# Kernel tuning notes

Measured on AMD Instinct MI355X. Metric: run time of the kernel, lower is better.

Reference implementation:

```python
import jax, jax.numpy as jnp
import numpy as np

PATCH = 8
EPS = 1e-5

def patch_split(x, s):
    # B C H W -> B s*s rH rW C
    B, C, H, W = x.shape
    rH, rW = H // s, W // s
    out = x.reshape(B, C, s, rH, s, rW)
    out = out.transpose(0, 2, 4, 3, 5, 1)
    return out.reshape(B, s * s, rH, rW, C)

def patch_recover(x, s):
    # B s*s rH rW C -> B C H W
    B, N, rH, rW, C = x.shape
    out = x.reshape(B, s, s, rH, rW, C)
    out = out.transpose(0, 5, 1, 3, 2, 4)
    return out.reshape(B, C, s * rH, s * rW)

def conv2d(x, w, pad):
    return jax.lax.conv_general_dilated(x, w, (1, 1), [(pad, pad), (pad, pad)],
                                        dimension_numbers=('NCHW', 'OIHW', 'NCHW'))

def bn_relu(x, g, b):
    # eval-mode BatchNorm2d with fresh running stats (mean=0, var=1)
    scale = (g / jnp.sqrt(1.0 + EPS))[None, :, None, None]
    return jax.nn.relu(x * scale + b[None, :, None, None])


def setup_inputs() -> dict:
    key = jax.random.key(0)
    ks = jax.random.split(key, 24)
    r = lambda i, shape, s=0.02: jax.random.normal(ks[i], shape, jnp.float32) * s
    B, H, W, C, K, P = 4, 64, 64, 512, 19, 64
    return {
        'M_1': jax.random.normal(ks[0], (B, 2048, H, W), jnp.float32),
        'F': jax.random.normal(ks[1], (B, C, H, W), jnp.float32),
        'I': jax.random.normal(ks[2], (B, K, H, W), jnp.float32),
        'R': jax.random.uniform(ks[3], (B, K, PATCH, PATCH), jnp.float32),
        'lg_w1': r(4, (P, P)), 'lg_w2': r(5, (C, C)),
        'fuse_w': r(6, (P,)), 'fuse_b': r(7, (1,)),
        'q_w': r(8, (256, C)), 'q_b': r(9, (256,)),
        'k_w': r(10, (256, C)), 'k_b': r(11, (256,)),
        'v_w': r(12, (256, C)), 'v_b': r(13, (256,)),
        'c1_w': r(14, (512, 256, 1, 1)),
        'bn1_g': jnp.ones((512,)), 'bn1_b': jnp.zeros((512,)),
        'c2_w': r(15, (512, 512, 3, 3)),
        'bn2_g': jnp.ones((512,)), 'bn2_b': jnp.zeros((512,)),
        'c3_w': r(16, (512, 2560, 3, 3)),
        'bn3_g': jnp.ones((512,)), 'bn3_b': jnp.zeros((512,)),
        'drop_w': r(17, (K, 512, 1, 1)),
    }


def reference(M_1, F, I, R, lg_w1, lg_w2, fuse_w, fuse_b, q_w, q_b, k_w, k_b,
              v_w, v_b, c1_w, bn1_g, bn1_b, c2_w, bn2_g, bn2_b, c3_w, bn3_g,
              bn3_b, drop_w):
    B = F.shape[0]
    F_p5 = patch_split(F, PATCH)          # B P rH rW C
    _, P, rH, rW, C = F_p5.shape
    I_p5 = patch_split(I, PATCH)          # B P rH rW K
    K = I_p5.shape[-1]
    F_p = F_p5.reshape(B, P, rH * rW, C)
    I_p = I_p5.reshape(B, P, rH * rW, K)
    bin_conf = R.reshape(B, K, P).transpose(0, 2, 1)[..., None]  # B P K 1
    pix = jax.nn.softmax(I_p, axis=2)
    F_l = jnp.einsum('bpnk,bpnc->bpkc', pix, F_p) * bin_conf     # B P K C
    # LG block: 1x1 conv over P channels, residual relu, linear over C
    h = jnp.einsum('qp,bpkc->bqkc', lg_w1, F_l)
    h = jax.nn.relu(h + F_l)
    F_l = jnp.einsum('bpkc,dc->bpkd', h, lg_w2)
    # FUSE: 1x1 conv P->1 (with bias); broadcast replaces torch .repeat
    F_g = jnp.einsum('p,bpkc->bkc', fuse_w, F_l) + fuse_b        # B K C
    query = jnp.einsum('bpnc,dc->bpnd', F_p, q_w) + q_b          # B P N 256
    key_ = jnp.einsum('bpkc,dc->bpkd', F_l, k_w) + k_b           # B P K 256
    value = jnp.einsum('bkc,dc->bkd', F_g, v_w) + v_b            # B K 256
    aff = jax.nn.softmax(jnp.einsum('bpnd,bpkd->bpnk', query, key_), axis=-1)
    F_s = jnp.einsum('bpnk,bkd->bpnd', aff, value)               # B P N 256
    F_s = patch_recover(F_s.reshape(B, P, rH, rW, -1), PATCH)    # B 256 H W
    Fo1 = F + bn_relu(conv2d(F_s, c1_w, 0), bn1_g, bn1_b)
    x2 = bn_relu(conv2d(Fo1, c2_w, 1), bn2_g, bn2_b)
    x3 = bn_relu(conv2d(jnp.concatenate([x2, M_1], axis=1), c3_w, 1), bn3_g, bn3_b)
    # Dropout2d is identity in eval; final 1x1 classifier conv
    return conv2d(x3, drop_w, 0)
```

## Files before the change

### kernel.cpp

```cpp
#include <hip/hip_runtime.h>
#include <hip/hip_bf16.h>

typedef __hip_bfloat16 bf16;
using short8 = __attribute__((ext_vector_type(8))) short;
using f32x4  = __attribute__((ext_vector_type(4))) float;

__device__ __forceinline__ float b2f(bf16 v){ return __bfloat162float(v); }
__device__ __forceinline__ bf16  f2b(float v){ return __float2bfloat16(v); }

#define EPSV 1e-5f

__device__ __forceinline__ void gload16(const void* g, void* l) {
  __builtin_amdgcn_global_load_lds(
      (const __attribute__((address_space(1))) unsigned int*)g,
      (__attribute__((address_space(3))) unsigned int*)l, 16, 0, 0);
}

__global__ __launch_bounds__(256) void k_cast(const float* __restrict__ in,
                                              bf16* __restrict__ out, int n4) {
  int i = blockIdx.x * 256 + threadIdx.x;
  if (i < n4) {
    float4 v = ((const float4*)in)[i];
    union { ushort4 u; bf16 h[4]; } o;
    o.h[0] = f2b(v.x); o.h[1] = f2b(v.y); o.h[2] = f2b(v.z); o.h[3] = f2b(v.w);
    ((ushort4*)out)[i] = o.u;
  }
}

__global__ __launch_bounds__(256) void k_wtr(const float* __restrict__ w,
                                             bf16* __restrict__ wt, int CI) {
  int oc = blockIdx.x, c0 = blockIdx.y * 128;
  __shared__ float ld[128 * 9];
  const float* src = w + ((size_t)oc * CI + c0) * 9;
  for (int i = threadIdx.x; i < 128 * 9; i += 256) ld[i] = src[i];
  __syncthreads();
  for (int i = threadIdx.x; i < 128 * 9; i += 256) {
    int k9 = i / 128, t = i - k9 * 128;
    wt[((size_t)k9 * 512 + oc) * CI + c0 + t] = f2b(ld[t * 9 + k9]);
  }
}

__global__ __launch_bounds__(256) void k_m1t(const float* __restrict__ M1,
                                             bf16* __restrict__ M1b) {
  int b = blockIdx.x >> 6, y = blockIdx.x & 63;
  int c0 = blockIdx.y * 64;
  __shared__ float t[64][65];
  for (int i = threadIdx.x; i < 4096; i += 256) {
    int cc = i >> 6, x = i & 63;
    t[x][cc] = M1[((size_t)(b * 2048 + c0 + cc) * 64 + y) * 64 + x];
  }
  __syncthreads();
  for (int i = threadIdx.x; i < 4096; i += 256) {
    int x = i >> 6, cc = i & 63;
    M1b[((size_t)((b * 64 + y) * 64 + x)) * 2048 + c0 + cc] = f2b(t[x][cc]);
  }
}

__global__ __launch_bounds__(256) void k_fp2(const float* __restrict__ F,
                                             bf16* __restrict__ FP) {
  int b = blockIdx.x >> 6, y = blockIdx.x & 63;
  int tid = threadIdx.x;
  __shared__ float t[256][65];
  int p_hi = (y >> 3) << 3, n_hi = (y & 7) << 3;
  for (int half = 0; half < 2; half++) {
    int c0 = half << 8;
    for (int i = tid; i < 256 * 64; i += 256) {
      int cc = i >> 6, x = i & 63;
      t[cc][x] = F[((size_t)(b * 512 + c0 + cc) * 64 + y) * 64 + x];
    }
    __syncthreads();
    for (int x = 0; x < 64; x++) {
      int p = p_hi + (x >> 3), n = n_hi + (x & 7);
      FP[((size_t)(b * 64 + p)) * 32768 + n * 512 + c0 + tid] = f2b(t[tid][x]);
    }
    __syncthreads();
  }
}

__global__ __launch_bounds__(256) void k_flocal2(const float* __restrict__ I,
        const float* __restrict__ R, const bf16* __restrict__ FP,
        float* __restrict__ FL0) {
  int bp = blockIdx.x, b = bp >> 6, p = bp & 63;
  int tid = threadIdx.x, w = tid >> 6, lane = tid & 63;
  __shared__ __align__(16) bf16 fps[64 * 512];
  __shared__ float pix[19][64];
  __shared__ float bc[19];
  {
    const bf16* src = FP + (size_t)bp * 32768 + lane * 8;
    #pragma unroll
    for (int t = 0; t < 16; t++) {
      int chunk = w + t * 4;
      gload16(src + chunk * 512, (char*)fps + chunk * 1024);
    }
  }
  int py = (p >> 3) * 8, px = (p & 7) * 8;
  for (int i = tid; i < 19 * 64; i += 256) {
    int k = i >> 6, n = i & 63;
    int y = py + (n >> 3), x = px + (n & 7);
    pix[k][n] = I[((size_t)(b * 19 + k) * 64 + y) * 64 + x];
  }
  if (tid < 19) bc[tid] = R[(size_t)(b * 19 + tid) * 64 + p];
  __syncthreads();
  if (tid < 19) {
    float mx = -1e30f;
    for (int n = 0; n < 64; n++) mx = fmaxf(mx, pix[tid][n]);
    float s = 0.f;
    for (int n = 0; n < 64; n++) { float e = __expf(pix[tid][n] - mx); pix[tid][n] = e; s += e; }
    float sc = bc[tid] / s;
    for (int n = 0; n < 64; n++) pix[tid][n] *= sc;
  }
  __syncthreads();
  for (int task = tid; task < 19 * 64; task += 256) {
    int k = task >> 6, c8 = (task & 63) << 3;
    float acc[8] = {};
    for (int n = 0; n < 64; n++) {
      float pv = pix[k][n];
      union { short8 s; bf16 h[8]; } v;
      v.s = *(const short8*)&fps[n * 512 + c8];
      #pragma unroll
      for (int j = 0; j < 8; j++) acc[j] += pv * b2f(v.h[j]);
    }
    float* dst = FL0 + ((size_t)(b * 64 + p) * 19 + k) * 512 + c8;
    #pragma unroll
    for (int j = 0; j < 8; j++) dst[j] = acc[j];
  }
}

__global__ __launch_bounds__(256) void k_lg1(const float* __restrict__ FL0,
        const float* __restrict__ w1, bf16* __restrict__ Hb) {
  int tid = threadIdx.x;
  int b = blockIdx.y;
  int n0 = blockIdx.x * 256;
  __shared__ float W[64][64];
  __shared__ float Xs[16][256];
  for (int i = tid; i < 4096; i += 256) W[i >> 6][i & 63] = w1[i];
  float acc[64];
  #pragma unroll
  for (int po = 0; po < 64; po++) acc[po] = 0.f;
  for (int q0 = 0; q0 < 64; q0 += 16) {
    __syncthreads();
    for (int i = tid; i < 4096; i += 256) {
      int q = i >> 8, j = i & 255;
      Xs[q][j] = FL0[(size_t)(b * 64 + q0 + q) * 9728 + n0 + j];
    }
    __syncthreads();
    for (int q = 0; q < 16; q++) {
      float xv = Xs[q][tid];
      #pragma unroll
      for (int po = 0; po < 64; po++) acc[po] += W[po][q0 + q] * xv;
    }
  }
  for (int po = 0; po < 64; po++) {
    float r = acc[po] + FL0[(size_t)(b * 64 + po) * 9728 + n0 + tid];
    Hb[(size_t)(b * 64 + po) * 9728 + n0 + tid] = f2b(fmaxf(r, 0.f));
  }
}

template<int MODE>
__global__ __launch_bounds__(256) void k_gmm(
    const bf16* __restrict__ A, const bf16* __restrict__ B,
    const float* __restrict__ bias, float* __restrict__ C,
    bf16* __restrict__ Cb, int N, int K,
    const float* __restrict__ g, const float* __restrict__ bb,
    const float* __restrict__ Fres, bf16* __restrict__ outb) {
  int tid = threadIdx.x;
  int m0 = blockIdx.x * 128, n0 = blockIdx.y * 128;
  int w = tid >> 6, lane = tid & 63, ln = lane & 15, qd = lane >> 4;
  int wm = w & 1, wn = w >> 1;
  __shared__ __align__(16) char smem[34816];

  f32x4 acc[4][4];
  #pragma unroll
  for (int i = 0; i < 4; i++)
    #pragma unroll
    for (int j = 0; j < 4; j++) acc[i][j] = (f32x4){0.f, 0.f, 0.f, 0.f};

  int rsub = lane >> 2, ch = lane & 3;
  auto stage = [&](int p) {
    char* base = smem + (p & 1) * 16384;
    int k0 = p << 5;
    #pragma unroll
    for (int t = 0; t < 2; t++) {
      int ii = w + t * 4;
      int r = ii * 16 + rsub;
      int sw = (ch ^ ((r >> 1) & 3)) << 3;
      gload16(A + (size_t)(m0 + r) * K + k0 + sw, base + ii * 1024);
      gload16(B + (size_t)(n0 + r) * K + k0 + sw, base + 8192 + ii * 1024);
    }
  };
  auto compute = [&](int p) {
    const char* base = smem + (p & 1) * 16384;
    short8 af[4], bv[4];
    #pragma unroll
    for (int mi = 0; mi < 4; mi++) {
      int r = wm * 64 + mi * 16 + ln;
      af[mi] = *(const short8*)(base + r * 64 + ((qd ^ ((r >> 1) & 3)) << 4));
    }
    #pragma unroll
    for (int ni = 0; ni < 4; ni++) {
      int r = wn * 64 + ni * 16 + ln;
      bv[ni] = *(const short8*)(base + 8192 + r * 64 + ((qd ^ ((r >> 1) & 3)) << 4));
    }
    #pragma unroll
    for (int mi = 0; mi < 4; mi++)
      #pragma unroll
      for (int ni = 0; ni < 4; ni++)
        acc[mi][ni] = __builtin_amdgcn_mfma_f32_16x16x32_bf16(
            af[mi], bv[ni], acc[mi][ni], 0, 0, 0);
  };

  int KT = K >> 5;
  stage(0);
  __syncthreads();
  for (int p = 0; p < KT; p++) {
    if (p + 1 < KT) stage(p + 1);
    compute(p);
    __syncthreads();
  }

  if (MODE <= 1) {
    #pragma unroll
    for (int mi = 0; mi < 4; mi++) {
      #pragma unroll
      for (int r = 0; r < 4; r++) {
        int m = m0 + wm * 64 + mi * 16 + qd * 4 + r;
        #pragma unroll
        for (int ni = 0; ni < 4; ni++) {
          int n = n0 + wn * 64 + ni * 16 + ln;
          float v = acc[mi][ni][r];
          if (bias) v += bias[n];
          C[(size_t)m * N + n] = v;
          if (MODE == 1) Cb[(size_t)m * N + n] = f2b(v);
        }
      }
    }
  } else {
    bf16* EP = (bf16*)smem;
    int b = n0 >> 12;
    #pragma unroll
    for (int mi = 0; mi < 4; mi++) {
      #pragma unroll
      for (int r = 0; r < 4; r++) {
        int ml = wm * 64 + mi * 16 + qd * 4 + r;
        int oc = m0 + ml;
        float sc = g[oc] * rsqrtf(1.f + EPSV);
        float bt = bb[oc];
        #pragma unroll
        for (int ni = 0; ni < 4; ni++) {
          int nl = wn * 64 + ni * 16 + ln;
          int pix = n0 + nl;
          int y = (pix >> 6) & 63, x = pix & 63;
          float v = fmaxf(acc[mi][ni][r] * sc + bt, 0.f)
                  + Fres[((size_t)(b * 512 + oc) * 64 + y) * 64 + x];
          EP[nl * 136 + ml] = f2b(v);
        }
      }
    }
    __syncthreads();
    int pl = tid >> 1, half = tid & 1;
    size_t gb = (size_t)(n0 + pl) * 512 + m0 + half * 64;
    const bf16* row = &EP[pl * 136 + half * 64];
    #pragma unroll
    for (int j2 = 0; j2 < 8; j2++)
      *(short8*)(outb + gb + j2 * 8) = *(const short8*)(row + j2 * 8);
  }
}

__global__ __launch_bounds__(256) void k_fusev(const float* __restrict__ FL,
        const float* __restrict__ fw, const float* __restrict__ fbv,
        const float* __restrict__ vw, const float* __restrict__ vb,
        float* __restrict__ VAL) {
  int tid = threadIdx.x;
  int bk = blockIdx.x, b = bk / 19, k = bk % 19;
  __shared__ float fwl[64];
  __shared__ __align__(16) float fg[512];
  if (tid < 64) fwl[tid] = fw[tid];
  __syncthreads();
  float fbias = fbv[0];
  for (int c = tid; c < 512; c += 256) {
    float s = 0.f;
    for (int p = 0; p < 64; p++)
      s += fwl[p] * FL[((size_t)(b * 64 + p) * 19 + k) * 512 + c];
    fg[c] = s + fbias;
  }
  __syncthreads();
  int d = tid;
  float s = vb[d];
  const float4* vr = (const float4*)(vw + (size_t)d * 512);
  const float4* fr = (const float4*)fg;
  for (int c4 = 0; c4 < 128; c4++) {
    float4 wv = vr[c4], f = fr[c4];
    s += f.x * wv.x + f.y * wv.y + f.z * wv.z + f.w * wv.w;
  }
  VAL[(size_t)bk * 256 + d] = s;
}

__global__ __launch_bounds__(256) void k_attn(const float* __restrict__ Q,
        const float* __restrict__ KEY, const float* __restrict__ VAL,
        bf16* __restrict__ FS) {
  int tid = threadIdx.x;
  int bp = blockIdx.x, b = bp >> 6, p = bp & 63;
  __shared__ __align__(16) float ks[19][256];
  __shared__ __align__(16) float vs[19][256];
  __shared__ float Ss[64][20];
  __shared__ bf16 ot[64][256];
  for (int i = tid; i < 19 * 256; i += 256) {
    ks[i >> 8][i & 255] = KEY[(size_t)bp * 19 * 256 + i];
    vs[i >> 8][i & 255] = VAL[(size_t)b * 19 * 256 + i];
  }
  __syncthreads();
  {
    int n = tid >> 2, kq = tid & 3;
    const float4* qrow = (const float4*)(Q + ((size_t)bp * 64 + n) * 256);
    for (int k = kq; k < 19; k += 4) {
      const float4* kr = (const float4*)&ks[k][0];
      float s = 0.f;
      for (int d4 = 0; d4 < 64; d4++) {
        float4 qv = qrow[d4], kv = kr[d4];
        s += qv.x * kv.x + qv.y * kv.y + qv.z * kv.z + qv.w * kv.w;
      }
      Ss[n][k] = s;
    }
  }
  __syncthreads();
  if (tid < 64) {
    float mx = -1e30f;
    for (int k = 0; k < 19; k++) mx = fmaxf(mx, Ss[tid][k]);
    float sum = 0.f;
    for (int k = 0; k < 19; k++) { float e = __expf(Ss[tid][k] - mx); Ss[tid][k] = e; sum += e; }
    float inv = 1.f / sum;
    for (int k = 0; k < 19; k++) Ss[tid][k] *= inv;
  }
  __syncthreads();
  {
    int d = tid;
    for (int nn = 0; nn < 64; nn++) {
      float s = 0.f;
      #pragma unroll
      for (int k = 0; k < 19; k++) s += Ss[nn][k] * vs[k][d];
      ot[nn][d] = f2b(s);
    }
  }
  __syncthreads();
  {
    int py = (p >> 3) * 8, px = (p & 7) * 8;
    int nn = tid >> 2, q = tid & 3;
    int y = py + (nn >> 3), x = px + (nn & 7);
    size_t gb = (((size_t)(b * 64 + y) * 64) + x) * 256 + q * 64;
    const bf16* row = &ot[nn][q * 64];
    #pragma unroll
    for (int j = 0; j < 8; j++)
      *(short8*)(FS + gb + j * 8) = *(const short8*)(row + j * 8);
  }
}

__global__ __launch_bounds__(256) void k_conv3(
    const bf16* __restrict__ Xin, int Cin,
    const bf16* __restrict__ M1b, const float* __restrict__ M1f, int C2,
    const bf16* __restrict__ WT,
    const float* __restrict__ g, const float* __restrict__ bb,
    bf16* __restrict__ out, int Cos) {
  int tid = threadIdx.x;
  int b = blockIdx.x >> 4, y0 = (blockIdx.x & 15) * 4;
  int oc0 = blockIdx.y * 128;
  int w = tid >> 6, lane = tid & 63, ln = lane & 15, qd = lane >> 4;
  int wocg = w & 1, wyp = w >> 1;
  int Ct = Cin + C2;

  __shared__ __align__(16) char smem[103936];
  char* smA  = smem;
  char* smB  = smem + 49152;
  char* dump = smem + 99840;

  for (int bufi = 0; bufi < 2; bufi++) {
    char* bbuf = smB + bufi * 25344;
    for (int i = tid; i < 6 * 2 * 32; i += 256) {
      int rl = i >> 6, hh = (i >> 5) & 1, kk = i & 31;
      *(bf16*)(bbuf + (rl * 66 + (hh ? 65 : 0)) * 64 + kk * 2) = f2b(0.f);
    }
    if (y0 == 0)
      for (int i = tid; i < 66 * 16; i += 256) ((float*)bbuf)[i] = 0.f;
    if (y0 == 60)
      for (int i = tid; i < 66 * 16; i += 256)
        ((float*)(bbuf + 5 * 66 * 64))[i] = 0.f;
  }

  f32x4 acc[4][8];
  #pragma unroll
  for (int i = 0; i < 4; i++)
    #pragma unroll
    for (int j = 0; j < 8; j++) acc[i][j] = (f32x4){0.f, 0.f, 0.f, 0.f};

  int NPH = (Ct >> 5) * 3;

  auto stageA = [&](int p) {
    int c0 = (p / 3) << 5, ky = p % 3;
    char* base = smA + (p & 1) * 24576;
    int j = w;
    #pragma unroll
    for (int t = 0; t < 6; t++, j += 4) {
      int kx = j >> 3, i8 = j & 7;
      int ocl = i8 * 16 + (lane >> 2);
      const bf16* src = WT + ((size_t)((ky * 3 + kx) * 512 + oc0 + ocl) * Ct + c0)
                      + (((lane & 3) ^ ((ocl >> 1) & 3)) << 3);
      gload16(src, base + (kx * 128 + i8 * 16) * 64);
    }
  };
  auto stageB = [&](int gi) {
    int c0 = gi << 5;
    char* bbuf = smB + (gi & 1) * 25344;
    if (c0 < Cin || M1b != nullptr) {
      const bf16* T; int Cs, cb;
      if (c0 < Cin) { T = Xin; Cs = Cin; cb = c0; }
      else          { T = M1b; Cs = C2;  cb = c0 - Cin; }
      #pragma unroll
      for (int rl = 0; rl < 6; rl++) {
        int yy = y0 + rl - 1;
        bool ok = (unsigned)yy < 64u;
        int yc = ok ? yy : y0;
        int xx = w * 16 + (lane >> 2), xr = xx + 1;
        const bf16* src = T + ((size_t)((b * 64 + yc) * 64 + xx) * Cs + cb)
                        + (((lane & 3) ^ ((xr >> 1) & 3)) << 3);
        char* dst = ok ? (bbuf + (rl * 66 + 1 + w * 16) * 64) : (dump + w * 1024);
        gload16(src, dst);
      }
    } else {
      #pragma unroll
      for (int t = 0; t < 2; t++) {
        int rl = w + t * 4;
        if (rl < 6) {
          int yy = y0 + rl - 1;
          if ((unsigned)yy < 64u) {
            int xx = lane, xr = xx + 1;
            const float* mp = M1f + ((size_t)(b * 2048 + (c0 - Cin)) * 64 + yy) * 64 + xx;
            #pragma unroll
            for (int q = 0; q < 8; q++) {
              union { ushort4 u; bf16 h[4]; } pk;
              #pragma unroll
              for (int jj = 0; jj < 4; jj++) pk.h[jj] = f2b(mp[(size_t)(q * 4 + jj) * 4096]);
              *(ushort4*)(bbuf + (rl * 66 + xr) * 64
                          + ((((q >> 1) ^ ((xr >> 1) & 3)) << 4) | ((q & 1) << 3))) = pk.u;
            }
          }
        }
      }
    }
  };
  auto computeP = [&](int p) {
    int ky = p % 3;
    const char* base = smA + (p & 1) * 24576;
    const char* bB   = smB + ((p / 3) & 1) * 25344;
    int rl0 = 2 * wyp + ky;
    #pragma unroll
    for (int kx = 0; kx < 3; kx++) {
      short8 af[4], bv[8];
      #pragma unroll
      for (int mi = 0; mi < 4; mi++) {
        int ocl = wocg * 64 + mi * 16 + ln;
        af[mi] = *(const short8*)(base + (kx * 128 + ocl) * 64
                                  + ((qd ^ ((ocl >> 1) & 3)) << 4));
      }
      #pragma unroll
      for (int ni = 0; ni < 8; ni++) {
        int rl = rl0 + (ni >> 2);
        int xr = (ni & 3) * 16 + ln + kx;
        bv[ni] = *(const short8*)(bB + (rl * 66 + xr) * 64
                                  + ((qd ^ ((xr >> 1) & 3)) << 4));
      }
      #pragma unroll
      for (int mi = 0; mi < 4; mi++)
        #pragma unroll
        for (int ni = 0; ni < 8; ni++)
          acc[mi][ni] = __builtin_amdgcn_mfma_f32_16x16x32_bf16(
              af[mi], bv[ni], acc[mi][ni], 0, 0, 0);
    }
  };

  stageB(0);
  stageA(0);
  asm volatile("s_waitcnt vmcnt(0)" ::: "memory");
  __syncthreads();

  for (int p = 0; p < NPH; p++) {
    int pn = p + 1;
    bool hasA = pn < NPH;
    bool hasB = hasA && (pn % 3 == 0);
    bool bfast = false;
    if (hasA) stageA(pn);
    if (hasB) {
      int gi = pn / 3;
      bfast = ((gi << 5) < Cin) || (M1b != nullptr);
      stageB(gi);
    }
    __builtin_amdgcn_sched_barrier(0);
    if (!hasA)              asm volatile("s_waitcnt vmcnt(0)"  ::: "memory");
    else if (hasB && bfast) asm volatile("s_waitcnt vmcnt(12)" ::: "memory");
    else                    asm volatile("s_waitcnt vmcnt(6)"  ::: "memory");
    __builtin_amdgcn_s_barrier();
    __builtin_amdgcn_sched_barrier(0);
    computeP(p);
    __builtin_amdgcn_sched_barrier(0);
    asm volatile("s_waitcnt lgkmcnt(0)" ::: "memory");
    __builtin_amdgcn_s_barrier();
  }
  __syncthreads();

  {
    bf16* EP = (bf16*)smem;
    #pragma unroll
    for (int mi = 0; mi < 4; mi++) {
      int oclb = wocg * 64 + mi * 16 + qd * 4;
      float sc[4], bt[4];
      #pragma unroll
      for (int r = 0; r < 4; r++) {
        int oc = oc0 + oclb + r;
        sc[r] = g[oc] * rsqrtf(1.f + EPSV);
        bt[r] = bb[oc];
      }
      #pragma unroll
      for (int ni = 0; ni < 8; ni++) {
        int yloc = 2 * wyp + (ni >> 2), x = (ni & 3) * 16 + ln;
        union { ushort4 u; bf16 h[4]; } pk;
        #pragma unroll
        for (int r = 0; r < 4; r++)
          pk.h[r] = f2b(fmaxf(acc[mi][ni][r] * sc[r] + bt[r], 0.f));
        *(ushort4*)&EP[(yloc * 64 + x) * 128 + oclb] = pk.u;
      }
    }
    __syncthreads();
    int p2 = tid >> 1, hh = tid & 1;
    #pragma unroll
    for (int pp = 0; pp < 2; pp++) {
      int pixl = pp * 128 + p2;
      int yloc = pixl >> 6, x = pixl & 63;
      size_t gb = ((size_t)((b * 64 + y0 + yloc) * 64 + x)) * Cos + oc0 + hh * 64;
      const bf16* row = &EP[pixl * 128 + hh * 64];
      #pragma unroll
      for (int k = 0; k < 8; k++)
        *(short8*)(out + gb + k * 8) = *(const short8*)(row + k * 8);
    }
  }
}

__global__ __launch_bounds__(256) void k_final(const bf16* __restrict__ X3,
        const float* __restrict__ dw, float* __restrict__ out) {
  int tid = threadIdx.x;
  int b = blockIdx.x >> 6, y = blockIdx.x & 63;
  __shared__ float W[19 * 512];
  for (int i = tid; i < 19 * 512; i += 256) W[i] = dw[i];
  __syncthreads();
  int x = tid & 63, kg = tid >> 6;
  const bf16* px = X3 + (((size_t)(b * 64 + y) * 64) + x) * 512;
  float acc[5] = {0.f, 0.f, 0.f, 0.f, 0.f};
  for (int c8 = 0; c8 < 512; c8 += 8) {
    union { short8 s; bf16 h[8]; } v;
    v.s = *(const short8*)(px + c8);
    float f[8];
    #pragma unroll
    for (int j = 0; j < 8; j++) f[j] = b2f(v.h[j]);
    #pragma unroll
    for (int i = 0; i < 5; i++) {
      int k = kg * 5 + i;
      if (k < 19) {
        const float* wr = &W[k * 512 + c8];
        #pragma unroll
        for (int j = 0; j < 8; j++) acc[i] += f[j] * wr[j];
      }
    }
  }
  for (int i = 0; i < 5; i++) {
    int k = kg * 5 + i;
    if (k < 19) out[((size_t)(b * 19 + k) * 64 + y) * 64 + x] = acc[i];
  }
}

extern "C" void kernel_launch(void* const* d_in, const int* in_sizes, int n_in,
                              void* d_out, int out_size, void* d_ws, size_t ws_size,
                              hipStream_t stream) {
  (void)in_sizes; (void)n_in; (void)out_size;
  const float* M1 = (const float*)d_in[0];
  const float* F  = (const float*)d_in[1];
  const float* Iin= (const float*)d_in[2];
  const float* R  = (const float*)d_in[3];
  const float* w1 = (const float*)d_in[4];
  const float* w2 = (const float*)d_in[5];
  const float* fw = (const float*)d_in[6];
  const float* fb = (const float*)d_in[7];
  const float* qw = (const float*)d_in[8];
  const float* qb = (const float*)d_in[9];
  const float* kw = (const float*)d_in[10];
  const float* kb = (const float*)d_in[11];
  const float* vw = (const float*)d_in[12];
  const float* vb = (const float*)d_in[13];
  const float* c1 = (const float*)d_in[14];
  const float* g1 = (const float*)d_in[15];
  const float* b1 = (const float*)d_in[16];
  const float* c2 = (const float*)d_in[17];
  const float* g2 = (const float*)d_in[18];
  const float* b2 = (const float*)d_in[19];
  const float* c3 = (const float*)d_in[20];
  const float* g3 = (const float*)d_in[21];
  const float* b3 = (const float*)d_in[22];
  const float* dw = (const float*)d_in[23];

  char* ws = (char*)d_ws;
  bool fast = ws_size >= (size_t)137363456ULL;

  bf16*  qwb  = (bf16*)(ws + 0);
  bf16*  kwb  = (bf16*)(ws + 262144);
  bf16*  w2b  = (bf16*)(ws + 524288);
  bf16*  c1b  = (bf16*)(ws + 1048576);
  bf16*  WT2  = (bf16*)(ws + 0);
  bf16*  WT3  = (bf16*)(ws + 4718592);
  bf16*  FS   = (bf16*)(ws + 28311552);
  bf16*  FO1  = (bf16*)(ws + 36700160);
  bf16*  X2   = (bf16*)(ws + 53477376);
  bf16*  M1bf = fast ? (bf16*)(ws + 70254592) : nullptr;
  bf16*  X3   = (bf16*)(ws + 28311552);
  bf16*  FP    = (bf16*) (ws + 53477376);
  float* QUERY = (float*)(ws + 70254592);
  float* FL0   = (float*)(ws + 87031808);
  bf16*  Hb    = (bf16*) (ws + 96993280);
  bf16*  FLb   = (bf16*) (ws + 101974016);
  float* KEY   = (float*)(ws + 106954752);
  float* VAL   = (float*)(ws + 111935488);
  float* FL    = FL0;

  k_cast<<<128, 256, 0, stream>>>(qw, qwb, 32768);
  k_cast<<<128, 256, 0, stream>>>(kw, kwb, 32768);
  k_cast<<<256, 256, 0, stream>>>(w2, w2b, 65536);
  k_cast<<<128, 256, 0, stream>>>(c1, c1b, 32768);
  k_fp2<<<256, 256, 0, stream>>>(F, FP);
  k_flocal2<<<256, 256, 0, stream>>>(Iin, R, FP, FL0);
  k_lg1<<<dim3(38, 4), 256, 0, stream>>>(FL0, w1, Hb);
  k_gmm<1><<<dim3(38, 4), 256, 0, stream>>>(Hb, w2b, nullptr, FL, FLb, 512, 512,
                                            nullptr, nullptr, nullptr, nullptr);
  k_fusev<<<76, 256, 0, stream>>>(FL, fw, fb, vw, vb, VAL);
  k_gmm<0><<<dim3(38, 2), 256, 0, stream>>>(FLb, kwb, kb, KEY, nullptr, 256, 512,
                                            nullptr, nullptr, nullptr, nullptr);
  k_gmm<0><<<dim3(128, 2), 256, 0, stream>>>(FP, qwb, qb, QUERY, nullptr, 256, 512,
                                             nullptr, nullptr, nullptr, nullptr);
  k_attn<<<256, 256, 0, stream>>>(QUERY, KEY, VAL, FS);
  if (fast) k_m1t<<<dim3(256, 32), 256, 0, stream>>>(M1, M1bf);
  k_gmm<2><<<dim3(4, 128), 256, 0, stream>>>(c1b, FS, nullptr, nullptr, nullptr,
                                             16384, 256, g1, b1, F, FO1);
  k_wtr<<<dim3(512, 4),  256, 0, stream>>>(c2, WT2, 512);
  k_wtr<<<dim3(512, 20), 256, 0, stream>>>(c3, WT3, 2560);
  k_conv3<<<dim3(64, 4), 256, 0, stream>>>(FO1, 512, nullptr, nullptr, 0,
                                           WT2, g2, b2, X2, 512);
  k_conv3<<<dim3(64, 4), 256, 0, stream>>>(X2, 512, M1bf, M1, 2048,
                                           WT3, g3, b3, X3, 512);
  k_final<<<256, 256, 0, stream>>>(X3, dw, (float*)d_out);
}
```

Before: 1.019 ms.

## Split conv3 tile across 8 waves instead of 4

```diff
diff --git a/kernel.cpp b/kernel.cpp
--- a/kernel.cpp
+++ b/kernel.cpp
@@ -354,7 +354,7 @@
   }
 }
 
-__global__ __launch_bounds__(256) void k_conv3(
+__global__ __launch_bounds__(512) void k_conv3(
     const bf16* __restrict__ Xin, int Cin,
     const bf16* __restrict__ M1b, const float* __restrict__ M1f, int C2,
     const bf16* __restrict__ WT,
@@ -367,38 +367,38 @@
   int wocg = w & 1, wyp = w >> 1;
   int Ct = Cin + C2;
 
-  __shared__ __align__(16) char smem[103936];
+  __shared__ __align__(16) char smem[100864];
   char* smA  = smem;
   char* smB  = smem + 49152;
   char* dump = smem + 99840;
 
   for (int bufi = 0; bufi < 2; bufi++) {
     char* bbuf = smB + bufi * 25344;
-    for (int i = tid; i < 6 * 2 * 32; i += 256) {
+    for (int i = tid; i < 6 * 2 * 32; i += 512) {
       int rl = i >> 6, hh = (i >> 5) & 1, kk = i & 31;
       *(bf16*)(bbuf + (rl * 66 + (hh ? 65 : 0)) * 64 + kk * 2) = f2b(0.f);
     }
     if (y0 == 0)
-      for (int i = tid; i < 66 * 16; i += 256) ((float*)bbuf)[i] = 0.f;
+      for (int i = tid; i < 66 * 16; i += 512) ((float*)bbuf)[i] = 0.f;
     if (y0 == 60)
-      for (int i = tid; i < 66 * 16; i += 256)
+      for (int i = tid; i < 66 * 16; i += 512)
         ((float*)(bbuf + 5 * 66 * 64))[i] = 0.f;
   }
 
-  f32x4 acc[4][8];
+  f32x4 acc[4][4];
   #pragma unroll
   for (int i = 0; i < 4; i++)
     #pragma unroll
-    for (int j = 0; j < 8; j++) acc[i][j] = (f32x4){0.f, 0.f, 0.f, 0.f};
+    for (int j = 0; j < 4; j++) acc[i][j] = (f32x4){0.f, 0.f, 0.f, 0.f};
 
   int NPH = (Ct >> 5) * 3;
 
   auto stageA = [&](int p) {
     int c0 = (p / 3) << 5, ky = p % 3;
     char* base = smA + (p & 1) * 24576;
-    int j = w;
-    #pragma unroll
-    for (int t = 0; t < 6; t++, j += 4) {
+    #pragma unroll
+    for (int t = 0; t < 3; t++) {
+      int j = w + t * 8;
       int kx = j >> 3, i8 = j & 7;
       int ocl = i8 * 16 + (lane >> 2);
       const bf16* src = WT + ((size_t)((ky * 3 + kx) * 512 + oc0 + ocl) * Ct + c0)
@@ -414,33 +414,31 @@
       if (c0 < Cin) { T = Xin; Cs = Cin; cb = c0; }
       else          { T = M1b; Cs = C2;  cb = c0 - Cin; }
       #pragma unroll
-      for (int rl = 0; rl < 6; rl++) {
+      for (int t = 0; t < 3; t++) {
+        int j = w + t * 8;
+        int rl = j >> 2, q = j & 3;
         int yy = y0 + rl - 1;
         bool ok = (unsigned)yy < 64u;
         int yc = ok ? yy : y0;
-        int xx = w * 16 + (lane >> 2), xr = xx + 1;
+        int xx = q * 16 + (lane >> 2), xr = xx + 1;
         const bf16* src = T + ((size_t)((b * 64 + yc) * 64 + xx) * Cs + cb)
                         + (((lane & 3) ^ ((xr >> 1) & 3)) << 3);
-        char* dst = ok ? (bbuf + (rl * 66 + 1 + w * 16) * 64) : (dump + w * 1024);
+        char* dst = ok ? (bbuf + (rl * 66 + 1 + q * 16) * 64) : dump;
         gload16(src, dst);
       }
     } else {
-      #pragma unroll
-      for (int t = 0; t < 2; t++) {
-        int rl = w + t * 4;
-        if (rl < 6) {
-          int yy = y0 + rl - 1;
-          if ((unsigned)yy < 64u) {
-            int xx = lane, xr = xx + 1;
-            const float* mp = M1f + ((size_t)(b * 2048 + (c0 - Cin)) * 64 + yy) * 64 + xx;
+      if (w < 6) {
+        int rl = w, yy = y0 + rl - 1;
+        if ((unsigned)yy < 64u) {
+          int xx = lane, xr = xx + 1;
+          const float* mp = M1f + ((size_t)(b * 2048 + (c0 - Cin)) * 64 + yy) * 64 + xx;
+          #pragma unroll
+          for (int q = 0; q < 8; q++) {
+            union { ushort4 u; bf16 h[4]; } pk;
             #pragma unroll
-            for (int q = 0; q < 8; q++) {
-              union { ushort4 u; bf16 h[4]; } pk;
-              #pragma unroll
-              for (int jj = 0; jj < 4; jj++) pk.h[jj] = f2b(mp[(size_t)(q * 4 + jj) * 4096]);
-              *(ushort4*)(bbuf + (rl * 66 + xr) * 64
-                          + ((((q >> 1) ^ ((xr >> 1) & 3)) << 4) | ((q & 1) << 3))) = pk.u;
-            }
+            for (int jj = 0; jj < 4; jj++) pk.h[jj] = f2b(mp[(size_t)(q * 4 + jj) * 4096]);
+            *(ushort4*)(bbuf + (rl * 66 + xr) * 64
+                        + ((((q >> 1) ^ ((xr >> 1) & 3)) << 4) | ((q & 1) << 3))) = pk.u;
           }
         }
       }
@@ -450,10 +448,10 @@
     int ky = p % 3;
     const char* base = smA + (p & 1) * 24576;
     const char* bB   = smB + ((p / 3) & 1) * 25344;
-    int rl0 = 2 * wyp + ky;
+    int rl = wyp + ky;
     #pragma unroll
     for (int kx = 0; kx < 3; kx++) {
-      short8 af[4], bv[8];
+      short8 af[4], bv[4];
       #pragma unroll
       for (int mi = 0; mi < 4; mi++) {
         int ocl = wocg * 64 + mi * 16 + ln;
@@ -461,16 +459,15 @@
                                   + ((qd ^ ((ocl >> 1) & 3)) << 4));
       }
       #pragma unroll
-      for (int ni = 0; ni < 8; ni++) {
-        int rl = rl0 + (ni >> 2);
-        int xr = (ni & 3) * 16 + ln + kx;
+      for (int ni = 0; ni < 4; ni++) {
+        int xr = ni * 16 + ln + kx;
         bv[ni] = *(const short8*)(bB + (rl * 66 + xr) * 64
                                   + ((qd ^ ((xr >> 1) & 3)) << 4));
       }
       #pragma unroll
       for (int mi = 0; mi < 4; mi++)
         #pragma unroll
-        for (int ni = 0; ni < 8; ni++)
+        for (int ni = 0; ni < 4; ni++)
           acc[mi][ni] = __builtin_amdgcn_mfma_f32_16x16x32_bf16(
               af[mi], bv[ni], acc[mi][ni], 0, 0, 0);
     }
@@ -493,9 +490,9 @@
       stageB(gi);
     }
     __builtin_amdgcn_sched_barrier(0);
-    if (!hasA)              asm volatile("s_waitcnt vmcnt(0)"  ::: "memory");
-    else if (hasB && bfast) asm volatile("s_waitcnt vmcnt(12)" ::: "memory");
-    else                    asm volatile("s_waitcnt vmcnt(6)"  ::: "memory");
+    if (!hasA)              asm volatile("s_waitcnt vmcnt(0)" ::: "memory");
+    else if (hasB && bfast) asm volatile("s_waitcnt vmcnt(6)" ::: "memory");
+    else                    asm volatile("s_waitcnt vmcnt(3)" ::: "memory");
     __builtin_amdgcn_s_barrier();
     __builtin_amdgcn_sched_barrier(0);
     computeP(p);
@@ -518,27 +515,23 @@
         bt[r] = bb[oc];
       }
       #pragma unroll
-      for (int ni = 0; ni < 8; ni++) {
-        int yloc = 2 * wyp + (ni >> 2), x = (ni & 3) * 16 + ln;
+      for (int ni = 0; ni < 4; ni++) {
+        int x = ni * 16 + ln;
         union { ushort4 u; bf16 h[4]; } pk;
         #pragma unroll
         for (int r = 0; r < 4; r++)
           pk.h[r] = f2b(fmaxf(acc[mi][ni][r] * sc[r] + bt[r], 0.f));
-        *(ushort4*)&EP[(yloc * 64 + x) * 128 + oclb] = pk.u;
+        *(ushort4*)&EP[(wyp * 64 + x) * 128 + oclb] = pk.u;
       }
     }
     __syncthreads();
-    int p2 = tid >> 1, hh = tid & 1;
-    #pragma unroll
-    for (int pp = 0; pp < 2; pp++) {
-      int pixl = pp * 128 + p2;
-      int yloc = pixl >> 6, x = pixl & 63;
-      size_t gb = ((size_t)((b * 64 + y0 + yloc) * 64 + x)) * Cos + oc0 + hh * 64;
-      const bf16* row = &EP[pixl * 128 + hh * 64];
-      #pragma unroll
-      for (int k = 0; k < 8; k++)
-        *(short8*)(out + gb + k * 8) = *(const short8*)(row + k * 8);
-    }
+    int pixl = tid >> 1, hh = tid & 1;
+    int yloc = pixl >> 6, x = pixl & 63;
+    size_t gb = ((size_t)((b * 64 + y0 + yloc) * 64 + x)) * Cos + oc0 + hh * 64;
+    const bf16* row = &EP[pixl * 128 + hh * 64];
+    #pragma unroll
+    for (int k = 0; k < 8; k++)
+      *(short8*)(out + gb + k * 8) = *(const short8*)(row + k * 8);
   }
 }
 
@@ -646,9 +639,9 @@
                                              16384, 256, g1, b1, F, FO1);
   k_wtr<<<dim3(512, 4),  256, 0, stream>>>(c2, WT2, 512);
   k_wtr<<<dim3(512, 20), 256, 0, stream>>>(c3, WT3, 2560);
-  k_conv3<<<dim3(64, 4), 256, 0, stream>>>(FO1, 512, nullptr, nullptr, 0,
+  k_conv3<<<dim3(64, 4), 512, 0, stream>>>(FO1, 512, nullptr, nullptr, 0,
                                            WT2, g2, b2, X2, 512);
-  k_conv3<<<dim3(64, 4), 256, 0, stream>>>(X2, 512, M1bf, M1, 2048,
+  k_conv3<<<dim3(64, 4), 512, 0, stream>>>(X2, 512, M1bf, M1, 2048,
                                            WT3, g3, b3, X3, 512);
   k_final<<<256, 256, 0, stream>>>(X3, dw, (float*)d_out);
 }
```

New measurement: 990.8 us. -2.7%, faster.
